# Optimization experiments

Hardware: AMD Instinct MI355X
Metric: run time of the kernel (lower is better)

The kernel has to match this reference:

```python
import jax, jax.numpy as jnp
import numpy as np

DIM = 256
HEADS = 8
HEAD_DIM = DIM // HEADS
SCALE = HEAD_DIM ** -0.5
EPS = 1e-5


def layer_norm(x, w, b):
    mu = jnp.mean(x, axis=-1, keepdims=True)
    var = jnp.mean(jnp.square(x - mu), axis=-1, keepdims=True)
    return (x - mu) * jax.lax.rsqrt(var + EPS) * w + b


def setup_inputs() -> dict:
    key = jax.random.key(0)
    ks = jax.random.split(key, 12)
    B, C, H, W = 2, DIM, 64, 64
    q_feat = jax.random.normal(ks[0], (B, C, H, W), dtype=jnp.float32)
    kv_feat = jax.random.normal(ks[1], (B, C, H, W), dtype=jnp.float32)
    s = 0.02
    return {
        "q_feat": q_feat,
        "kv_feat": kv_feat,
        "norm_q_w": jnp.ones((C,), jnp.float32),
        "norm_q_b": jnp.zeros((C,), jnp.float32),
        "norm_kv_w": jnp.ones((C,), jnp.float32),
        "norm_kv_b": jnp.zeros((C,), jnp.float32),
        "wq": jax.random.normal(ks[2], (C, C), jnp.float32) * s,
        "bq": jnp.zeros((C,), jnp.float32),
        "wk": jax.random.normal(ks[3], (C, C), jnp.float32) * s,
        "bk": jnp.zeros((C,), jnp.float32),
        "wv": jax.random.normal(ks[4], (C, C), jnp.float32) * s,
        "bv": jnp.zeros((C,), jnp.float32),
        "wp": jax.random.normal(ks[5], (C, C), jnp.float32) * s,
        "bp": jnp.zeros((C,), jnp.float32),
    }


def reference(q_feat, kv_feat, norm_q_w, norm_q_b, norm_kv_w, norm_kv_b,
              wq, bq, wk, bk, wv, bv, wp, bp):
    B, C, H, W = q_feat.shape
    N = H * W
    # N > max_tokens(256) -> avg_pool2d(k=2,s=2) on kv (H,W even so no ceil padding)
    kv = kv_feat.reshape(B, C, H // 2, 2, W // 2, 2).mean(axis=(3, 5))
    Hk, Wk = kv.shape[2], kv.shape[3]
    Nk = Hk * Wk
    q = q_feat.transpose(0, 2, 3, 1).reshape(B, N, C)
    kv = kv.transpose(0, 2, 3, 1).reshape(B, Nk, C)
    q = layer_norm(q, norm_q_w, norm_q_b)
    kv = layer_norm(kv, norm_kv_w, norm_kv_b)
    # projections (weights stored as (out,in) like torch Linear: x @ W.T + b)
    qh = (q @ wq.T + bq).reshape(B, N, HEADS, HEAD_DIM).transpose(0, 2, 1, 3)
    kh = (kv @ wk.T + bk).reshape(B, Nk, HEADS, HEAD_DIM).transpose(0, 2, 1, 3)
    vh = (kv @ wv.T + bv).reshape(B, Nk, HEADS, HEAD_DIM).transpose(0, 2, 1, 3)
    attn = jnp.einsum("bhnd,bhmd->bhnm", qh * SCALE, kh)
    attn = jax.nn.softmax(attn, axis=-1)
    out = jnp.einsum("bhnm,bhmd->bhnd", attn, vh)
    out = out.transpose(0, 2, 1, 3).reshape(B, N, C)
    out = out @ wp.T + bp
    return out.reshape(B, H, W, C).transpose(0, 3, 1, 2)
```

## Files before the change

### kernel.cpp

```cpp
#include <hip/hip_runtime.h>


#define CDIM   256
#define NTOK   4096
#define NKTOK  1024
#define HDIM   32
#define QSCALE 0.2550530290582177f
#define LN_EPS 1e-5f

typedef __attribute__((ext_vector_type(8))) short bf16x8;
typedef __attribute__((ext_vector_type(4))) float f32x4;
typedef __attribute__((ext_vector_type(4))) uint u32x4;

__device__ __forceinline__ ushort f2bf(float f) {
  uint u = __builtin_bit_cast(uint, f);
  u += 0x7fff + ((u >> 16) & 1);
  return (ushort)(u >> 16);
}

__device__ __forceinline__ float fast_exp2(float x) {
  float r;
  asm("v_exp_f32 %0, %1" : "=v"(r) : "v"(x));
  return r;
}

__device__ __forceinline__ uint cvt_pk_bf16(float lo, float hi) {
  uint r;
  asm("v_cvt_pk_bf16_f32 %0, %1, %2" : "=v"(r) : "v"(lo), "v"(hi));
  return r;
}

__device__ __forceinline__ void gload_lds16(const void* g, void* l) {
  __builtin_amdgcn_global_load_lds(
      (const __attribute__((address_space(1))) unsigned int*)g,
      (__attribute__((address_space(3))) unsigned int*)l, 16, 0, 0);
}

__global__ __launch_bounds__(256) void prep_kernel(
    const float* __restrict__ q_feat, const float* __restrict__ kv_feat,
    const float* __restrict__ nqw, const float* __restrict__ nqb,
    const float* __restrict__ nkw, const float* __restrict__ nkb,
    const float* __restrict__ wq, const float* __restrict__ wk,
    const float* __restrict__ wvv, const float* __restrict__ wp,
    ushort* __restrict__ wq_bf, ushort* __restrict__ wk_bf,
    ushort* __restrict__ wv_bf, ushort* __restrict__ wp_bf,
    ushort* __restrict__ q_ln, ushort* __restrict__ kv_ln) {
  __shared__ float preds[2][256];
  __shared__ float pstat[2][32];
  const int bid = blockIdx.x;
  const int tid = threadIdx.x;

  if (bid < 256) {
    const int mat = bid >> 6;
    const int base = (bid & 63) * 1024 + tid * 4;
    const float* s; ushort* d;
    switch (mat) {
      case 0: s = wq; d = wq_bf; break;
      case 1: s = wk; d = wk_bf; break;
      case 2: s = wvv; d = wv_bf; break;
      default: s = wp; d = wp_bf; break;
    }
    const float4 v = *reinterpret_cast<const float4*>(s + base);
    uint2 pk;
    pk.x = (uint)f2bf(v.x) | ((uint)f2bf(v.y) << 16);
    pk.y = (uint)f2bf(v.z) | ((uint)f2bf(v.w) << 16);
    *reinterpret_cast<uint2*>(d + base) = pk;
    return;
  }

  if (bid < 768) {
    const int tok = tid & 15, cg = tid >> 4;
    const int T = (bid - 256) * 16 + tok;
    const int b = T >> 12, n = T & 4095;
    const float* src = q_feat + ((size_t)b * CDIM + cg * 16) * NTOK + n;
    float vals[16];
    float s = 0.f, ss = 0.f;
#pragma unroll
    for (int ci = 0; ci < 16; ++ci) {
      const float v = src[(size_t)ci * NTOK];
      vals[ci] = v;
      s += v; ss = fmaf(v, v, ss);
    }
    preds[0][cg * 16 + tok] = s;
    preds[1][cg * 16 + tok] = ss;
    __syncthreads();
    if (tid < 16) {
      float st = 0.f, sst = 0.f;
#pragma unroll
      for (int k = 0; k < 16; ++k) { st += preds[0][k * 16 + tid]; sst += preds[1][k * 16 + tid]; }
      const float mu = st * (1.f / 256.f);
      const float var = sst * (1.f / 256.f) - mu * mu;
      pstat[0][tid] = mu;
      pstat[1][tid] = rsqrtf(var + LN_EPS);
    }
    __syncthreads();
    const float mu = pstat[0][tok];
    const float rs = pstat[1][tok];
    ushort* dst = q_ln + (size_t)T * CDIM + cg * 16;
#pragma unroll
    for (int ci = 0; ci < 16; ci += 4) {
      ushort h[4];
#pragma unroll
      for (int j = 0; j < 4; ++j) {
        const int c = cg * 16 + ci + j;
        h[j] = f2bf(fmaf((vals[ci + j] - mu) * rs, nqw[c], nqb[c]));
      }
      uint2 pk;
      pk.x = (uint)h[0] | ((uint)h[1] << 16);
      pk.y = (uint)h[2] | ((uint)h[3] << 16);
      *reinterpret_cast<uint2*>(dst + ci) = pk;
    }
    return;
  }

  {
    const int tok = tid & 7, cg = tid >> 3;
    const int T = (bid - 768) * 8 + tok;
    const int b = T >> 10, nk = T & 1023;
    const int hk = nk >> 5, wk2 = nk & 31;
    const float* src = kv_feat + ((size_t)b * CDIM + cg * 8) * NTOK + hk * 128 + wk2 * 2;
    float vals[8];
    float s = 0.f, ss = 0.f;
#pragma unroll
    for (int ci = 0; ci < 8; ++ci) {
      const float* p = src + (size_t)ci * NTOK;
      const float2 r0 = *reinterpret_cast<const float2*>(p);
      const float2 r1 = *reinterpret_cast<const float2*>(p + 64);
      const float v = 0.25f * ((r0.x + r0.y) + (r1.x + r1.y));
      vals[ci] = v;
      s += v; ss = fmaf(v, v, ss);
    }
    preds[0][cg * 8 + tok] = s;
    preds[1][cg * 8 + tok] = ss;
    __syncthreads();
    if (tid < 8) {
      float st = 0.f, sst = 0.f;
#pragma unroll
      for (int k = 0; k < 32; ++k) { st += preds[0][k * 8 + tid]; sst += preds[1][k * 8 + tid]; }
      const float mu = st * (1.f / 256.f);
      const float var = sst * (1.f / 256.f) - mu * mu;
      pstat[0][tid] = mu;
      pstat[1][tid] = rsqrtf(var + LN_EPS);
    }
    __syncthreads();
    const float mu = pstat[0][tok];
    const float rs = pstat[1][tok];
    ushort* dst = kv_ln + (size_t)T * CDIM + cg * 8;
#pragma unroll
    for (int ci = 0; ci < 8; ci += 4) {
      ushort h[4];
#pragma unroll
      for (int j = 0; j < 4; ++j) {
        const int c = cg * 8 + ci + j;
        h[j] = f2bf(fmaf((vals[ci + j] - mu) * rs, nkw[c], nkb[c]));
      }
      uint2 pk;
      pk.x = (uint)h[0] | ((uint)h[1] << 16);
      pk.y = (uint)h[2] | ((uint)h[3] << 16);
      *reinterpret_cast<uint2*>(dst + ci) = pk;
    }
  }
}

__global__ __launch_bounds__(256) void qkv_kernel(
    const ushort* __restrict__ q_ln, const ushort* __restrict__ kv_ln,
    const ushort* __restrict__ wq_bf, const ushort* __restrict__ wk_bf,
    const ushort* __restrict__ wv_bf,
    const float* __restrict__ bq, const float* __restrict__ bk,
    const float* __restrict__ bv,
    ushort* __restrict__ Qp, ushort* __restrict__ kvp) {
  const int bid = blockIdx.x;
  int seg, sb;
  const ushort *X, *W; const float* bias;
  if (bid < 256)      { seg = 0; sb = bid;       X = q_ln;  W = wq_bf; bias = bq; }
  else if (bid < 320) { seg = 1; sb = bid - 256; X = kv_ln; W = wk_bf; bias = bk; }
  else                { seg = 2; sb = bid - 320; X = kv_ln; W = wv_bf; bias = bv; }

  const int lane = threadIdx.x & 63;
  const int wvi = threadIdx.x >> 6;
  const int nlan = lane & 15, g = lane >> 4;
  const int rowgrp = wvi >> 1, colh = wvi & 1;
  const int r0 = sb * 32 + rowgrp * 16;

  f32x4 acc[8];
#pragma unroll
  for (int nt = 0; nt < 8; ++nt) acc[nt] = (f32x4){0.f, 0.f, 0.f, 0.f};

  const ushort* xp = X + (size_t)(r0 + nlan) * CDIM + g * 8;
  const ushort* wp = W + (size_t)(colh * 128 + nlan) * CDIM + g * 8;
#pragma unroll
  for (int k0 = 0; k0 < 8; ++k0) {
    const bf16x8 a = *reinterpret_cast<const bf16x8*>(xp + k0 * 32);
#pragma unroll
    for (int nt = 0; nt < 8; ++nt) {
      const bf16x8 bfr = *reinterpret_cast<const bf16x8*>(wp + (size_t)nt * 16 * CDIM + k0 * 32);
      acc[nt] = __builtin_amdgcn_mfma_f32_16x16x32_bf16(a, bfr, acc[nt], 0, 0, 0);
    }
  }

#pragma unroll
  for (int nt = 0; nt < 8; ++nt) {
    const int j = colh * 128 + nt * 16 + nlan;
    const float bj = bias[j];
#pragma unroll
    for (int reg = 0; reg < 4; ++reg) {
      const int r = r0 + 4 * g + reg;
      const float v = acc[nt][reg] + bj;
      if (seg == 0) {
        Qp[(size_t)r * CDIM + j] = f2bf(v * QSCALE);
      } else if (seg == 1) {
        const int bb = r >> 10, k = r & 1023;
        const int kc = k >> 7, kk = k & 127;
        const int m = kk >> 5, w = kk & 31;
        const int t = 2 * m + ((w >> 2) & 1);
        const int rr = ((w >> 3) << 2) | (w & 3);
        const int hh = j >> 5, d = j & 31;
        kvp[(((size_t)((bb * 8 + hh) * 8 + kc) * 16 + t) << 9) +
            ((d >> 3) * 16 + rr) * 8 + (d & 7)] = f2bf(v);
      } else {
        const int bb = r >> 10, mk = r & 1023;
        const int hh = j >> 5, d = j & 31;
        const int dt = d >> 4, rr = d & 15;
        const int kc = mk >> 7, km = mk & 127;
        const int ks = km >> 5, w = km & 31;
        const int gq = w >> 3, jj = w & 7;
        kvp[(((size_t)((bb * 8 + hh) * 8 + kc) * 16 + (8 + dt * 4 + ks)) << 9) +
            (gq * 16 + rr) * 8 + jj] = f2bf(v);
      }
    }
  }
}

__global__ __launch_bounds__(256) void attn_kernel(const ushort* __restrict__ Qp,
                                                   const ushort* __restrict__ kvp,
                                                   ushort* __restrict__ aout) {
  __shared__ __align__(16) ushort kvf[2][16][512];
  const int lane = threadIdx.x & 63;
  const int wvi = threadIdx.x >> 6;
  const int nlan = lane & 15, g = lane >> 4;
  const int bh = blockIdx.y;
  const int b = bh >> 3, h = bh & 7;
  const int n0 = blockIdx.x * 128 + wvi * 32;

  bf16x8 qf[2];
#pragma unroll
  for (int qt = 0; qt < 2; ++qt)
    qf[qt] = *reinterpret_cast<const bf16x8*>(
        Qp + (size_t)(b * NTOK + n0 + qt * 16 + nlan) * CDIM + h * HDIM + g * 8);

  const ushort* kvb = kvp + ((size_t)bh << 16);

  auto stage = [&](int buf, int kc_idx) {
    const ushort* cb = kvb + ((size_t)kc_idx << 13);
#pragma unroll
    for (int i = 0; i < 4; ++i) {
      const int t = wvi * 4 + i;
      gload_lds16(cb + t * 512 + lane * 8, &kvf[buf][t][0]);
    }
  };

  f32x4 acc[2][2];
#pragma unroll
  for (int qt = 0; qt < 2; ++qt) {
    acc[qt][0] = (f32x4){0.f, 0.f, 0.f, 0.f};
    acc[qt][1] = (f32x4){0.f, 0.f, 0.f, 0.f};
  }
  float lsum[2] = {0.f, 0.f};
  const f32x4 zero = {0.f, 0.f, 0.f, 0.f};

  stage(0, 0);
  for (int c = 0; c < 8; ++c) {
    const int buf = c & 1;
    __syncthreads();
    if (c < 7) stage(buf ^ 1, c + 1);

#pragma unroll
    for (int m = 0; m < 4; ++m) {
      uint pk[2][4];
#pragma unroll
      for (int half = 0; half < 2; ++half) {
        const bf16x8 kf = *reinterpret_cast<const bf16x8*>(&kvf[buf][2 * m + half][lane * 8]);
#pragma unroll
        for (int qt = 0; qt < 2; ++qt) {
          const f32x4 s = __builtin_amdgcn_mfma_f32_16x16x32_bf16(kf, qf[qt], zero, 0, 0, 0);
          const float p0 = fast_exp2(s[0]), p1 = fast_exp2(s[1]);
          const float p2 = fast_exp2(s[2]), p3 = fast_exp2(s[3]);
          lsum[qt] += (p0 + p1) + (p2 + p3);
          pk[qt][half * 2 + 0] = cvt_pk_bf16(p0, p1);
          pk[qt][half * 2 + 1] = cvt_pk_bf16(p2, p3);
        }
      }
#pragma unroll
      for (int qt = 0; qt < 2; ++qt) {
        const u32x4 w = {pk[qt][0], pk[qt][1], pk[qt][2], pk[qt][3]};
        const bf16x8 af = __builtin_bit_cast(bf16x8, w);
#pragma unroll
        for (int dt = 0; dt < 2; ++dt) {
          const bf16x8 vf = *reinterpret_cast<const bf16x8*>(&kvf[buf][8 + dt * 4 + m][lane * 8]);
          acc[qt][dt] = __builtin_amdgcn_mfma_f32_16x16x32_bf16(af, vf, acc[qt][dt], 0, 0, 0);
        }
      }
    }
  }

#pragma unroll
  for (int qt = 0; qt < 2; ++qt) {
    lsum[qt] += __shfl_xor(lsum[qt], 16);
    lsum[qt] += __shfl_xor(lsum[qt], 32);
  }

  ushort* dst = aout + (size_t)(b * NTOK + n0) * CDIM + h * HDIM;
#pragma unroll
  for (int qt = 0; qt < 2; ++qt) {
#pragma unroll
    for (int reg = 0; reg < 4; ++reg) {
      const float inv = 1.f / __shfl(lsum[qt], 4 * g + reg);
      const size_t row = (size_t)(qt * 16 + 4 * g + reg) * CDIM;
      dst[row + nlan] = f2bf(acc[qt][0][reg] * inv);
      dst[row + 16 + nlan] = f2bf(acc[qt][1][reg] * inv);
    }
  }
}

__global__ __launch_bounds__(256) void outproj_kernel(const ushort* __restrict__ A,
                                                      const ushort* __restrict__ W,
                                                      const float* __restrict__ bias,
                                                      float* __restrict__ out) {
  __shared__ float ts[256][33];
  const int lane = threadIdx.x & 63;
  const int wvi = threadIdx.x >> 6;
  const int nlan = lane & 15, g = lane >> 4;
  const int rowgrp = wvi >> 1, colh = wvi & 1;
  const int r0b = blockIdx.x * 32;
  const int r0 = r0b + rowgrp * 16;

  f32x4 acc[8];
#pragma unroll
  for (int nt = 0; nt < 8; ++nt) acc[nt] = (f32x4){0.f, 0.f, 0.f, 0.f};

  const ushort* xp = A + (size_t)(r0 + nlan) * CDIM + g * 8;
  const ushort* wp = W + (size_t)(colh * 128 + nlan) * CDIM + g * 8;
#pragma unroll
  for (int k0 = 0; k0 < 8; ++k0) {
    const bf16x8 a = *reinterpret_cast<const bf16x8*>(xp + k0 * 32);
#pragma unroll
    for (int nt = 0; nt < 8; ++nt) {
      const bf16x8 bfr = *reinterpret_cast<const bf16x8*>(wp + (size_t)nt * 16 * CDIM + k0 * 32);
      acc[nt] = __builtin_amdgcn_mfma_f32_16x16x32_bf16(a, bfr, acc[nt], 0, 0, 0);
    }
  }

#pragma unroll
  for (int nt = 0; nt < 8; ++nt) {
    const int j = colh * 128 + nt * 16 + nlan;
    const float bj = bias[j];
#pragma unroll
    for (int reg = 0; reg < 4; ++reg)
      ts[j][rowgrp * 16 + 4 * g + reg] = acc[nt][reg] + bj;
  }
  __syncthreads();
  const int b = r0b >> 12;
  const int n0g = r0b & 4095;
#pragma unroll
  for (int k = 0; k < 32; ++k) {
    const int idx = k * 256 + threadIdx.x;
    const int cl = idx >> 5, tok = idx & 31;
    out[((size_t)b * CDIM + cl) * NTOK + n0g + tok] = ts[cl][tok];
  }
}

extern "C" void kernel_launch(void* const* d_in, const int* in_sizes, int n_in,
                              void* d_out, int out_size, void* d_ws, size_t ws_size,
                              hipStream_t stream) {
  (void)in_sizes; (void)n_in; (void)out_size; (void)ws_size;
  const float* q_feat  = (const float*)d_in[0];
  const float* kv_feat = (const float*)d_in[1];
  const float* nqw = (const float*)d_in[2];
  const float* nqb = (const float*)d_in[3];
  const float* nkw = (const float*)d_in[4];
  const float* nkb = (const float*)d_in[5];
  const float* wq  = (const float*)d_in[6];
  const float* bq  = (const float*)d_in[7];
  const float* wk  = (const float*)d_in[8];
  const float* bk  = (const float*)d_in[9];
  const float* wv  = (const float*)d_in[10];
  const float* bv  = (const float*)d_in[11];
  const float* wp  = (const float*)d_in[12];
  const float* bp  = (const float*)d_in[13];
  float* out = (float*)d_out;

  ushort* p = (ushort*)d_ws;
  ushort* wq_bf = p; p += 65536;
  ushort* wk_bf = p; p += 65536;
  ushort* wv_bf = p; p += 65536;
  ushort* wp_bf = p; p += 65536;
  ushort* q_ln  = p; p += 8192 * 256;
  ushort* kv_ln = p; p += 2048 * 256;
  ushort* Qp    = p; p += 8192 * 256;
  ushort* kvp   = p; p += 16 * 8 * 16 * 512;
  ushort* aout  = p; p += 8192 * 256;

  prep_kernel<<<1024, 256, 0, stream>>>(q_feat, kv_feat, nqw, nqb, nkw, nkb,
                                        wq, wk, wv, wp,
                                        wq_bf, wk_bf, wv_bf, wp_bf, q_ln, kv_ln);
  qkv_kernel<<<384, 256, 0, stream>>>(q_ln, kv_ln, wq_bf, wk_bf, wv_bf,
                                      bq, bk, bv, Qp, kvp);
  attn_kernel<<<dim3(32, 16), 256, 0, stream>>>(Qp, kvp, aout);
  outproj_kernel<<<256, 256, 0, stream>>>(aout, wp_bf, bp, out);
}
```

Baseline: 62.16 us.

## Load K/V fragments directly from global into registers, halve per-wave query tile

Removes the LDS double-buffered staging and __syncthreads in the attention kernel. Each wave now prefetches K and V fragments from global memory into registers, two steps ahead. Each wave processes 16 query rows instead of 32, and the grid is doubled to 64x16 blocks for more parallelism. This trades barrier and LDS overhead for more global/L2 reads, since K/V reuse across query tiles within a wave is lost.

```diff
diff --git a/kernel.cpp b/kernel.cpp
--- a/kernel.cpp
+++ b/kernel.cpp
@@ -28,12 +28,6 @@
   uint r;
   asm("v_cvt_pk_bf16_f32 %0, %1, %2" : "=v"(r) : "v"(lo), "v"(hi));
   return r;
-}
-
-__device__ __forceinline__ void gload_lds16(const void* g, void* l) {
-  __builtin_amdgcn_global_load_lds(
-      (const __attribute__((address_space(1))) unsigned int*)g,
-      (__attribute__((address_space(3))) unsigned int*)l, 16, 0, 0);
 }
 
 __global__ __launch_bounds__(256) void prep_kernel(
@@ -234,91 +228,72 @@
 __global__ __launch_bounds__(256) void attn_kernel(const ushort* __restrict__ Qp,
                                                    const ushort* __restrict__ kvp,
                                                    ushort* __restrict__ aout) {
-  __shared__ __align__(16) ushort kvf[2][16][512];
   const int lane = threadIdx.x & 63;
   const int wvi = threadIdx.x >> 6;
   const int nlan = lane & 15, g = lane >> 4;
   const int bh = blockIdx.y;
   const int b = bh >> 3, h = bh & 7;
-  const int n0 = blockIdx.x * 128 + wvi * 32;
-
-  bf16x8 qf[2];
-#pragma unroll
-  for (int qt = 0; qt < 2; ++qt)
-    qf[qt] = *reinterpret_cast<const bf16x8*>(
-        Qp + (size_t)(b * NTOK + n0 + qt * 16 + nlan) * CDIM + h * HDIM + g * 8);
-
-  const ushort* kvb = kvp + ((size_t)bh << 16);
-
-  auto stage = [&](int buf, int kc_idx) {
-    const ushort* cb = kvb + ((size_t)kc_idx << 13);
-#pragma unroll
-    for (int i = 0; i < 4; ++i) {
-      const int t = wvi * 4 + i;
-      gload_lds16(cb + t * 512 + lane * 8, &kvf[buf][t][0]);
-    }
+  const int n0 = blockIdx.x * 64 + wvi * 16;
+
+  const bf16x8 qf = *reinterpret_cast<const bf16x8*>(
+      Qp + (size_t)(b * NTOK + n0 + nlan) * CDIM + h * HDIM + g * 8);
+
+  const ushort* kvb = kvp + ((size_t)bh << 16) + lane * 8;
+
+  auto kaddr = [&](int mk, int half) {
+    return reinterpret_cast<const bf16x8*>(
+        kvb + ((mk >> 2) << 13) + (((mk & 3) * 2 + half) << 9));
   };
-
-  f32x4 acc[2][2];
-#pragma unroll
-  for (int qt = 0; qt < 2; ++qt) {
-    acc[qt][0] = (f32x4){0.f, 0.f, 0.f, 0.f};
-    acc[qt][1] = (f32x4){0.f, 0.f, 0.f, 0.f};
-  }
-  float lsum[2] = {0.f, 0.f};
+  auto vaddr = [&](int mk, int dt) {
+    return reinterpret_cast<const bf16x8*>(
+        kvb + ((mk >> 2) << 13) + ((8 + dt * 4 + (mk & 3)) << 9));
+  };
+
+  f32x4 acc0 = {0.f, 0.f, 0.f, 0.f}, acc1 = {0.f, 0.f, 0.f, 0.f};
+  float lsum = 0.f;
   const f32x4 zero = {0.f, 0.f, 0.f, 0.f};
 
-  stage(0, 0);
-  for (int c = 0; c < 8; ++c) {
-    const int buf = c & 1;
-    __syncthreads();
-    if (c < 7) stage(buf ^ 1, c + 1);
-
-#pragma unroll
-    for (int m = 0; m < 4; ++m) {
-      uint pk[2][4];
-#pragma unroll
-      for (int half = 0; half < 2; ++half) {
-        const bf16x8 kf = *reinterpret_cast<const bf16x8*>(&kvf[buf][2 * m + half][lane * 8]);
-#pragma unroll
-        for (int qt = 0; qt < 2; ++qt) {
-          const f32x4 s = __builtin_amdgcn_mfma_f32_16x16x32_bf16(kf, qf[qt], zero, 0, 0, 0);
-          const float p0 = fast_exp2(s[0]), p1 = fast_exp2(s[1]);
-          const float p2 = fast_exp2(s[2]), p3 = fast_exp2(s[3]);
-          lsum[qt] += (p0 + p1) + (p2 + p3);
-          pk[qt][half * 2 + 0] = cvt_pk_bf16(p0, p1);
-          pk[qt][half * 2 + 1] = cvt_pk_bf16(p2, p3);
-        }
-      }
-#pragma unroll
-      for (int qt = 0; qt < 2; ++qt) {
-        const u32x4 w = {pk[qt][0], pk[qt][1], pk[qt][2], pk[qt][3]};
-        const bf16x8 af = __builtin_bit_cast(bf16x8, w);
-#pragma unroll
-        for (int dt = 0; dt < 2; ++dt) {
-          const bf16x8 vf = *reinterpret_cast<const bf16x8*>(&kvf[buf][8 + dt * 4 + m][lane * 8]);
-          acc[qt][dt] = __builtin_amdgcn_mfma_f32_16x16x32_bf16(af, vf, acc[qt][dt], 0, 0, 0);
-        }
-      }
-    }
-  }
-
-#pragma unroll
-  for (int qt = 0; qt < 2; ++qt) {
-    lsum[qt] += __shfl_xor(lsum[qt], 16);
-    lsum[qt] += __shfl_xor(lsum[qt], 32);
-  }
+  auto compute = [&](const bf16x8& k0, const bf16x8& k1,
+                     const bf16x8& v0, const bf16x8& v1) {
+    const f32x4 s0 = __builtin_amdgcn_mfma_f32_16x16x32_bf16(k0, qf, zero, 0, 0, 0);
+    const f32x4 s1 = __builtin_amdgcn_mfma_f32_16x16x32_bf16(k1, qf, zero, 0, 0, 0);
+    const float p0 = fast_exp2(s0[0]), p1 = fast_exp2(s0[1]);
+    const float p2 = fast_exp2(s0[2]), p3 = fast_exp2(s0[3]);
+    const float p4 = fast_exp2(s1[0]), p5 = fast_exp2(s1[1]);
+    const float p6 = fast_exp2(s1[2]), p7 = fast_exp2(s1[3]);
+    lsum += ((p0 + p1) + (p2 + p3)) + ((p4 + p5) + (p6 + p7));
+    const u32x4 w = {cvt_pk_bf16(p0, p1), cvt_pk_bf16(p2, p3),
+                     cvt_pk_bf16(p4, p5), cvt_pk_bf16(p6, p7)};
+    const bf16x8 af = __builtin_bit_cast(bf16x8, w);
+    acc0 = __builtin_amdgcn_mfma_f32_16x16x32_bf16(af, v0, acc0, 0, 0, 0);
+    acc1 = __builtin_amdgcn_mfma_f32_16x16x32_bf16(af, v1, acc1, 0, 0, 0);
+  };
+
+  bf16x8 kA0 = *kaddr(0, 0), kA1 = *kaddr(0, 1);
+  bf16x8 vA0 = *vaddr(0, 0), vA1 = *vaddr(0, 1);
+  bf16x8 kB0, kB1, vB0, vB1;
+#pragma unroll 1
+  for (int mk = 0; mk < 32; mk += 2) {
+    kB0 = *kaddr(mk + 1, 0); kB1 = *kaddr(mk + 1, 1);
+    vB0 = *vaddr(mk + 1, 0); vB1 = *vaddr(mk + 1, 1);
+    compute(kA0, kA1, vA0, vA1);
+    if (mk + 2 < 32) {
+      kA0 = *kaddr(mk + 2, 0); kA1 = *kaddr(mk + 2, 1);
+      vA0 = *vaddr(mk + 2, 0); vA1 = *vaddr(mk + 2, 1);
+    }
+    compute(kB0, kB1, vB0, vB1);
+  }
+
+  lsum += __shfl_xor(lsum, 16);
+  lsum += __shfl_xor(lsum, 32);
 
   ushort* dst = aout + (size_t)(b * NTOK + n0) * CDIM + h * HDIM;
 #pragma unroll
-  for (int qt = 0; qt < 2; ++qt) {
-#pragma unroll
-    for (int reg = 0; reg < 4; ++reg) {
-      const float inv = 1.f / __shfl(lsum[qt], 4 * g + reg);
-      const size_t row = (size_t)(qt * 16 + 4 * g + reg) * CDIM;
-      dst[row + nlan] = f2bf(acc[qt][0][reg] * inv);
-      dst[row + 16 + nlan] = f2bf(acc[qt][1][reg] * inv);
-    }
+  for (int reg = 0; reg < 4; ++reg) {
+    const float inv = 1.f / __shfl(lsum, 4 * g + reg);
+    const size_t row = (size_t)(4 * g + reg) * CDIM;
+    dst[row + nlan] = f2bf(acc0[reg] * inv);
+    dst[row + 16 + nlan] = f2bf(acc1[reg] * inv);
   }
 }
 
@@ -405,6 +380,6 @@
                                         wq_bf, wk_bf, wv_bf, wp_bf, q_ln, kv_ln);
   qkv_kernel<<<384, 256, 0, stream>>>(q_ln, kv_ln, wq_bf, wk_bf, wv_bf,
                                       bq, bk, bv, Qp, kvp);
-  attn_kernel<<<dim3(32, 16), 256, 0, stream>>>(Qp, kvp, aout);
+  attn_kernel<<<dim3(64, 16), 256, 0, stream>>>(Qp, kvp, aout);
   outproj_kernel<<<256, 256, 0, stream>>>(aout, wp_bf, bp, out);
 }
```

Measured after the change: 65.11 us. 1.05x slower.

## Fuse avg-pool and LayerNorm into QKV projection kernel via LDS staging

Applied to the files above, without the earlier changes.

Moves the LayerNorm (and kv avg-pool) computation from the prep kernel into the QKV projection kernel, which normalizes a 32-token tile and stages it in LDS as bf16 before the MFMA loop. This removes the q_ln/kv_ln global round trip (write and re-read of about 5 MB bf16). The prep kernel now only converts weights. In exchange each QKV block does more serial work before its MFMAs, holds 32 floats per thread in registers, and uses extra LDS, which may reduce occupancy. The 384-block grid gives less parallelism for the LN loads than the old 768 LN blocks had.

```diff
diff --git a/kernel.cpp b/kernel.cpp
--- a/kernel.cpp
+++ b/kernel.cpp
@@ -37,160 +37,121 @@
 }
 
 __global__ __launch_bounds__(256) void prep_kernel(
+    const float* __restrict__ wq, const float* __restrict__ wk,
+    const float* __restrict__ wvv, const float* __restrict__ wp,
+    ushort* __restrict__ wq_bf, ushort* __restrict__ wk_bf,
+    ushort* __restrict__ wv_bf, ushort* __restrict__ wp_bf) {
+  const int bid = blockIdx.x;
+  const int mat = bid >> 6;
+  const int base = (bid & 63) * 1024 + threadIdx.x * 4;
+  const float* s; ushort* d;
+  switch (mat) {
+    case 0: s = wq; d = wq_bf; break;
+    case 1: s = wk; d = wk_bf; break;
+    case 2: s = wvv; d = wv_bf; break;
+    default: s = wp; d = wp_bf; break;
+  }
+  const float4 v = *reinterpret_cast<const float4*>(s + base);
+  uint2 pk;
+  pk.x = (uint)f2bf(v.x) | ((uint)f2bf(v.y) << 16);
+  pk.y = (uint)f2bf(v.z) | ((uint)f2bf(v.w) << 16);
+  *reinterpret_cast<uint2*>(d + base) = pk;
+}
+
+__global__ __launch_bounds__(256) void qkv_kernel(
     const float* __restrict__ q_feat, const float* __restrict__ kv_feat,
     const float* __restrict__ nqw, const float* __restrict__ nqb,
     const float* __restrict__ nkw, const float* __restrict__ nkb,
-    const float* __restrict__ wq, const float* __restrict__ wk,
-    const float* __restrict__ wvv, const float* __restrict__ wp,
-    ushort* __restrict__ wq_bf, ushort* __restrict__ wk_bf,
-    ushort* __restrict__ wv_bf, ushort* __restrict__ wp_bf,
-    ushort* __restrict__ q_ln, ushort* __restrict__ kv_ln) {
-  __shared__ float preds[2][256];
-  __shared__ float pstat[2][32];
-  const int bid = blockIdx.x;
-  const int tid = threadIdx.x;
-
-  if (bid < 256) {
-    const int mat = bid >> 6;
-    const int base = (bid & 63) * 1024 + tid * 4;
-    const float* s; ushort* d;
-    switch (mat) {
-      case 0: s = wq; d = wq_bf; break;
-      case 1: s = wk; d = wk_bf; break;
-      case 2: s = wvv; d = wv_bf; break;
-      default: s = wp; d = wp_bf; break;
-    }
-    const float4 v = *reinterpret_cast<const float4*>(s + base);
-    uint2 pk;
-    pk.x = (uint)f2bf(v.x) | ((uint)f2bf(v.y) << 16);
-    pk.y = (uint)f2bf(v.z) | ((uint)f2bf(v.w) << 16);
-    *reinterpret_cast<uint2*>(d + base) = pk;
-    return;
-  }
-
-  if (bid < 768) {
-    const int tok = tid & 15, cg = tid >> 4;
-    const int T = (bid - 256) * 16 + tok;
-    const int b = T >> 12, n = T & 4095;
-    const float* src = q_feat + ((size_t)b * CDIM + cg * 16) * NTOK + n;
-    float vals[16];
-    float s = 0.f, ss = 0.f;
-#pragma unroll
-    for (int ci = 0; ci < 16; ++ci) {
-      const float v = src[(size_t)ci * NTOK];
-      vals[ci] = v;
-      s += v; ss = fmaf(v, v, ss);
-    }
-    preds[0][cg * 16 + tok] = s;
-    preds[1][cg * 16 + tok] = ss;
-    __syncthreads();
-    if (tid < 16) {
-      float st = 0.f, sst = 0.f;
-#pragma unroll
-      for (int k = 0; k < 16; ++k) { st += preds[0][k * 16 + tid]; sst += preds[1][k * 16 + tid]; }
-      const float mu = st * (1.f / 256.f);
-      const float var = sst * (1.f / 256.f) - mu * mu;
-      pstat[0][tid] = mu;
-      pstat[1][tid] = rsqrtf(var + LN_EPS);
-    }
-    __syncthreads();
-    const float mu = pstat[0][tok];
-    const float rs = pstat[1][tok];
-    ushort* dst = q_ln + (size_t)T * CDIM + cg * 16;
-#pragma unroll
-    for (int ci = 0; ci < 16; ci += 4) {
-      ushort h[4];
-#pragma unroll
-      for (int j = 0; j < 4; ++j) {
-        const int c = cg * 16 + ci + j;
-        h[j] = f2bf(fmaf((vals[ci + j] - mu) * rs, nqw[c], nqb[c]));
-      }
-      uint2 pk;
-      pk.x = (uint)h[0] | ((uint)h[1] << 16);
-      pk.y = (uint)h[2] | ((uint)h[3] << 16);
-      *reinterpret_cast<uint2*>(dst + ci) = pk;
-    }
-    return;
-  }
-
-  {
-    const int tok = tid & 7, cg = tid >> 3;
-    const int T = (bid - 768) * 8 + tok;
-    const int b = T >> 10, nk = T & 1023;
-    const int hk = nk >> 5, wk2 = nk & 31;
-    const float* src = kv_feat + ((size_t)b * CDIM + cg * 8) * NTOK + hk * 128 + wk2 * 2;
-    float vals[8];
-    float s = 0.f, ss = 0.f;
-#pragma unroll
-    for (int ci = 0; ci < 8; ++ci) {
-      const float* p = src + (size_t)ci * NTOK;
-      const float2 r0 = *reinterpret_cast<const float2*>(p);
-      const float2 r1 = *reinterpret_cast<const float2*>(p + 64);
-      const float v = 0.25f * ((r0.x + r0.y) + (r1.x + r1.y));
-      vals[ci] = v;
-      s += v; ss = fmaf(v, v, ss);
-    }
-    preds[0][cg * 8 + tok] = s;
-    preds[1][cg * 8 + tok] = ss;
-    __syncthreads();
-    if (tid < 8) {
-      float st = 0.f, sst = 0.f;
-#pragma unroll
-      for (int k = 0; k < 32; ++k) { st += preds[0][k * 8 + tid]; sst += preds[1][k * 8 + tid]; }
-      const float mu = st * (1.f / 256.f);
-      const float var = sst * (1.f / 256.f) - mu * mu;
-      pstat[0][tid] = mu;
-      pstat[1][tid] = rsqrtf(var + LN_EPS);
-    }
-    __syncthreads();
-    const float mu = pstat[0][tok];
-    const float rs = pstat[1][tok];
-    ushort* dst = kv_ln + (size_t)T * CDIM + cg * 8;
-#pragma unroll
-    for (int ci = 0; ci < 8; ci += 4) {
-      ushort h[4];
-#pragma unroll
-      for (int j = 0; j < 4; ++j) {
-        const int c = cg * 8 + ci + j;
-        h[j] = f2bf(fmaf((vals[ci + j] - mu) * rs, nkw[c], nkb[c]));
-      }
-      uint2 pk;
-      pk.x = (uint)h[0] | ((uint)h[1] << 16);
-      pk.y = (uint)h[2] | ((uint)h[3] << 16);
-      *reinterpret_cast<uint2*>(dst + ci) = pk;
-    }
-  }
-}
-
-__global__ __launch_bounds__(256) void qkv_kernel(
-    const ushort* __restrict__ q_ln, const ushort* __restrict__ kv_ln,
     const ushort* __restrict__ wq_bf, const ushort* __restrict__ wk_bf,
     const ushort* __restrict__ wv_bf,
     const float* __restrict__ bq, const float* __restrict__ bk,
     const float* __restrict__ bv,
     ushort* __restrict__ Qp, ushort* __restrict__ kvp) {
+  __shared__ ushort xs[32][264];
+  __shared__ float red[2][256];
+  __shared__ float stat[2][32];
+
   const int bid = blockIdx.x;
   int seg, sb;
-  const ushort *X, *W; const float* bias;
-  if (bid < 256)      { seg = 0; sb = bid;       X = q_ln;  W = wq_bf; bias = bq; }
-  else if (bid < 320) { seg = 1; sb = bid - 256; X = kv_ln; W = wk_bf; bias = bk; }
-  else                { seg = 2; sb = bid - 320; X = kv_ln; W = wv_bf; bias = bv; }
-
-  const int lane = threadIdx.x & 63;
-  const int wvi = threadIdx.x >> 6;
+  const ushort* W; const float* bias;
+  if (bid < 256)      { seg = 0; sb = bid;       W = wq_bf; bias = bq; }
+  else if (bid < 320) { seg = 1; sb = bid - 256; W = wk_bf; bias = bk; }
+  else                { seg = 2; sb = bid - 320; W = wv_bf; bias = bv; }
+
+  const int tid = threadIdx.x;
+  const int tok = tid & 31, cg = tid >> 5;
+  const int r0g = sb * 32;
+
+  float vals[32];
+  float s = 0.f, ss = 0.f;
+  if (seg == 0) {
+    const int b = r0g >> 12;
+    const int n = (r0g & 4095) + tok;
+    const float* src = q_feat + (size_t)(b * CDIM + cg * 32) * NTOK + n;
+#pragma unroll
+    for (int ci = 0; ci < 32; ++ci) {
+      const float v = src[(size_t)ci * NTOK];
+      vals[ci] = v; s += v; ss = fmaf(v, v, ss);
+    }
+  } else {
+    const int b = r0g >> 10;
+    const int hk = (r0g & 1023) >> 5;
+    const float* src = kv_feat + (size_t)(b * CDIM + cg * 32) * NTOK + hk * 128 + tok * 2;
+#pragma unroll
+    for (int ci = 0; ci < 32; ++ci) {
+      const float* p = src + (size_t)ci * NTOK;
+      const float2 a0 = *reinterpret_cast<const float2*>(p);
+      const float2 a1 = *reinterpret_cast<const float2*>(p + 64);
+      const float v = 0.25f * ((a0.x + a0.y) + (a1.x + a1.y));
+      vals[ci] = v; s += v; ss = fmaf(v, v, ss);
+    }
+  }
+  red[0][tid] = s; red[1][tid] = ss;
+  __syncthreads();
+  if (tid < 32) {
+    float st = 0.f, sst = 0.f;
+#pragma unroll
+    for (int k = 0; k < 8; ++k) { st += red[0][k * 32 + tid]; sst += red[1][k * 32 + tid]; }
+    const float mu = st * (1.f / 256.f);
+    const float var = sst * (1.f / 256.f) - mu * mu;
+    stat[0][tid] = mu; stat[1][tid] = rsqrtf(var + LN_EPS);
+  }
+  __syncthreads();
+  {
+    const float mu = stat[0][tok], rs = stat[1][tok];
+    const float* lw = (seg == 0) ? nqw : nkw;
+    const float* lb = (seg == 0) ? nqb : nkb;
+#pragma unroll
+    for (int ci = 0; ci < 32; ci += 4) {
+      ushort h[4];
+#pragma unroll
+      for (int j2 = 0; j2 < 4; ++j2) {
+        const int c = cg * 32 + ci + j2;
+        h[j2] = f2bf(fmaf((vals[ci + j2] - mu) * rs, lw[c], lb[c]));
+      }
+      uint2 pk2;
+      pk2.x = (uint)h[0] | ((uint)h[1] << 16);
+      pk2.y = (uint)h[2] | ((uint)h[3] << 16);
+      *reinterpret_cast<uint2*>(&xs[tok][cg * 32 + ci]) = pk2;
+    }
+  }
+  __syncthreads();
+
+  const int lane = tid & 63;
+  const int wvi = tid >> 6;
   const int nlan = lane & 15, g = lane >> 4;
   const int rowgrp = wvi >> 1, colh = wvi & 1;
-  const int r0 = sb * 32 + rowgrp * 16;
+  const int lrow = rowgrp * 16 + nlan;
+  const int r0 = r0g + rowgrp * 16;
 
   f32x4 acc[8];
 #pragma unroll
   for (int nt = 0; nt < 8; ++nt) acc[nt] = (f32x4){0.f, 0.f, 0.f, 0.f};
 
-  const ushort* xp = X + (size_t)(r0 + nlan) * CDIM + g * 8;
   const ushort* wp = W + (size_t)(colh * 128 + nlan) * CDIM + g * 8;
 #pragma unroll
   for (int k0 = 0; k0 < 8; ++k0) {
-    const bf16x8 a = *reinterpret_cast<const bf16x8*>(xp + k0 * 32);
+    const bf16x8 a = *reinterpret_cast<const bf16x8*>(&xs[lrow][g * 8 + k0 * 32]);
 #pragma unroll
     for (int nt = 0; nt < 8; ++nt) {
       const bf16x8 bfr = *reinterpret_cast<const bf16x8*>(wp + (size_t)nt * 16 * CDIM + k0 * 32);
@@ -394,17 +355,13 @@
   ushort* wk_bf = p; p += 65536;
   ushort* wv_bf = p; p += 65536;
   ushort* wp_bf = p; p += 65536;
-  ushort* q_ln  = p; p += 8192 * 256;
-  ushort* kv_ln = p; p += 2048 * 256;
   ushort* Qp    = p; p += 8192 * 256;
   ushort* kvp   = p; p += 16 * 8 * 16 * 512;
   ushort* aout  = p; p += 8192 * 256;
 
-  prep_kernel<<<1024, 256, 0, stream>>>(q_feat, kv_feat, nqw, nqb, nkw, nkb,
-                                        wq, wk, wv, wp,
-                                        wq_bf, wk_bf, wv_bf, wp_bf, q_ln, kv_ln);
-  qkv_kernel<<<384, 256, 0, stream>>>(q_ln, kv_ln, wq_bf, wk_bf, wv_bf,
-                                      bq, bk, bv, Qp, kvp);
+  prep_kernel<<<256, 256, 0, stream>>>(wq, wk, wv, wp, wq_bf, wk_bf, wv_bf, wp_bf);
+  qkv_kernel<<<384, 256, 0, stream>>>(q_feat, kv_feat, nqw, nqb, nkw, nkb,
+                                      wq_bf, wk_bf, wv_bf, bq, bk, bv, Qp, kvp);
   attn_kernel<<<dim3(32, 16), 256, 0, stream>>>(Qp, kvp, aout);
   outproj_kernel<<<256, 256, 0, stream>>>(aout, wp_bf, bp, out);
 }
```

Result: no change. 62.33 us (+0.3%).
